# Kernel tuning notes

Measured on AMD Instinct MI355X. Metric: run time of the kernel, lower is better.

The kernel has to match this reference:

```python
import jax, jax.numpy as jnp
import numpy as np

IN_DIM = 1024
OUT_DIM = 1024
QK_DIM = OUT_DIM // 4  # 256


def setup_inputs() -> dict:
    key = jax.random.key(0)
    kx, ky, kq, kk, kv = jax.random.split(key, 5)
    B, Sq, Sk = 16, 2048, 2048
    x = jax.random.normal(kx, (B, Sq, IN_DIM), dtype=jnp.float32)
    y = jax.random.normal(ky, (B, Sk, IN_DIM), dtype=jnp.float32)
    s = 1.0 / np.sqrt(IN_DIM)
    Wq = jax.random.normal(kq, (IN_DIM, QK_DIM), dtype=jnp.float32) * s
    Wk = jax.random.normal(kk, (IN_DIM, QK_DIM), dtype=jnp.float32) * s
    Wv = jax.random.normal(kv, (IN_DIM, OUT_DIM), dtype=jnp.float32) * s
    return {"x": x, "y": y, "Wq": Wq, "Wk": Wk, "Wv": Wv}


def reference(x, y, Wq, Wk, Wv):
    # q: [B,Sq,dk], k: [B,Sk,dk]
    q = jnp.einsum("bsd,dk->bsk", x, Wq)
    k = jnp.einsum("btd,dk->btk", y, Wk)
    # NOTE: original scales by out_dim**0.5, not qk dim
    scores = jnp.einsum("bsk,btk->bst", q, k) / jnp.sqrt(jnp.float32(OUT_DIM))
    attn = jax.nn.softmax(scores, axis=-1)
    v = jnp.einsum("btd,de->bte", y, Wv)
    out = jnp.einsum("bst,bte->bse", attn, v)
    return out + x
```

## Files before the change

### kernel.cpp

```cpp
#include <hip/hip_runtime.h>

typedef __attribute__((ext_vector_type(8))) short bf16x8;
typedef __attribute__((ext_vector_type(4))) short s16x4;
typedef __attribute__((ext_vector_type(4))) float f32x4;

#define MFMA16(a,b,c) __builtin_amdgcn_mfma_f32_16x16x32_bf16((a),(b),(c),0,0,0)

__device__ __forceinline__ unsigned short f2bf(float f) {
  unsigned int u = __float_as_uint(f);
  return (unsigned short)((u + 0x7fffu + ((u >> 16) & 1u)) >> 16);
}
__device__ __forceinline__ float bf2f(unsigned short u) {
  return __uint_as_float(((unsigned int)u) << 16);
}

__device__ __forceinline__ void gload16(const void* g, void* l) {
  __builtin_amdgcn_global_load_lds((const __attribute__((address_space(1))) void*)g,
                                   (__attribute__((address_space(3))) void*)l, 16, 0, 0);
}

__global__ __launch_bounds__(256) void cvt_bf16(const float* __restrict__ in,
                                                unsigned short* __restrict__ out, int n8) {
  for (int i = blockIdx.x * 256 + threadIdx.x; i < n8; i += gridDim.x * 256) {
    float4 a = ((const float4*)in)[2 * i];
    float4 b = ((const float4*)in)[2 * i + 1];
    s16x4 p0, p1;
    p0[0] = f2bf(a.x); p0[1] = f2bf(a.y); p0[2] = f2bf(a.z); p0[3] = f2bf(a.w);
    p1[0] = f2bf(b.x); p1[1] = f2bf(b.y); p1[2] = f2bf(b.z); p1[3] = f2bf(b.w);
    ((s16x4*)out)[2 * i] = p0;
    ((s16x4*)out)[2 * i + 1] = p1;
  }
}

__global__ __launch_bounds__(256) void tcvt(const float* __restrict__ W,
                                            unsigned short* __restrict__ Wt, int K, int N) {
  __shared__ float t[32][33];
  const int n0 = blockIdx.x * 32, k0 = blockIdx.y * 32;
  const int c = threadIdx.x & 31, r8 = threadIdx.x >> 5;
#pragma unroll
  for (int p = 0; p < 4; ++p) {
    int r = r8 + p * 8;
    t[r][c] = W[(size_t)(k0 + r) * N + n0 + c];
  }
  __syncthreads();
#pragma unroll
  for (int p = 0; p < 4; ++p) {
    int r = r8 + p * 8;
    Wt[(size_t)(n0 + r) * K + k0 + c] = f2bf(t[c][r]);
  }
}

__global__ __launch_bounds__(256) void proj_gemm(
    const unsigned short* __restrict__ A, const unsigned short* __restrict__ Bt,
    void* __restrict__ Cv, int N, int mode, float scale)
{
  __shared__ __align__(16) unsigned short As[2][4096];
  __shared__ __align__(16) unsigned short Bs[2][4096];
  const int tid = threadIdx.x, lane = tid & 63, w = tid >> 6;
  const int wr = w >> 1, wc = w & 1;
  const int lrow = lane & 15, lg = lane >> 4;
  const size_t bm = (size_t)blockIdx.x * 128;
  const size_t bn = (size_t)blockIdx.y * 128;
  const int rl = lane >> 2, cq = lane & 3;

  auto stage = [&](int kt, int buf) {
#pragma unroll
    for (int u = 0; u < 2; ++u) {
      int row = w * 32 + u * 16 + rl;
      gload16(A  + (bm + row) * 1024 + kt * 32 + cq * 8, &As[buf][(w * 32 + u * 16) * 32]);
      gload16(Bt + (bn + row) * 1024 + kt * 32 + cq * 8, &Bs[buf][(w * 32 + u * 16) * 32]);
    }
  };

  f32x4 acc[4][4] = {};
  stage(0, 0);
  __syncthreads();

  for (int kt = 0; kt < 32; ++kt) {
    const int cur = kt & 1;
    if (kt + 1 < 32) stage(kt + 1, cur ^ 1);
    bf16x8 af[4], bfr[4];
#pragma unroll
    for (int i = 0; i < 4; ++i)
      af[i] = *(const bf16x8*)&As[cur][(wr * 64 + i * 16 + lrow) * 32 + lg * 8];
#pragma unroll
    for (int j = 0; j < 4; ++j)
      bfr[j] = *(const bf16x8*)&Bs[cur][(wc * 64 + j * 16 + lrow) * 32 + lg * 8];
    __builtin_amdgcn_s_setprio(1);
#pragma unroll
    for (int i = 0; i < 4; ++i)
#pragma unroll
      for (int j = 0; j < 4; ++j)
        acc[i][j] = MFMA16(af[i], bfr[j], acc[i][j]);
    __builtin_amdgcn_s_setprio(0);
    __syncthreads();
  }

  const int orow0 = blockIdx.x * 128 + wr * 64;
  const int ocol0 = blockIdx.y * 128 + wc * 64;
  if (mode == 0) {
    unsigned short* C = (unsigned short*)Cv;
#pragma unroll
    for (int i = 0; i < 4; ++i)
#pragma unroll
      for (int j = 0; j < 4; ++j) {
        int col = ocol0 + j * 16 + lrow;
#pragma unroll
        for (int r = 0; r < 4; ++r) {
          int row = orow0 + i * 16 + lg * 4 + r;
          C[(size_t)row * N + col] = f2bf(acc[i][j][r] * scale);
        }
      }
  } else {
    unsigned char* C8 = (unsigned char*)Cv;
#pragma unroll
    for (int i = 0; i < 4; ++i) {
      int m0 = orow0 + i * 16 + lg * 4;
      int bb = m0 >> 11, t = m0 & 2047;
      int tw = t >> 6, t64 = t & 63;
#pragma unroll
      for (int j = 0; j < 4; ++j) {
        int e = ocol0 + j * 16 + lrow;
        int eg = e >> 4;
        int pk = 0;
        pk = __builtin_amdgcn_cvt_pk_fp8_f32(acc[i][j][0], acc[i][j][1], pk, false);
        pk = __builtin_amdgcn_cvt_pk_fp8_f32(acc[i][j][2], acc[i][j][3], pk, true);
        *(unsigned int*)(C8 + (size_t)bb * 2097152
                            + ((size_t)(eg * 32 + tw)) * 1024 + lrow * 64 + t64)
            = (unsigned int)pk;
      }
    }
  }
}

#define SBAR  do { __builtin_amdgcn_s_barrier(); __builtin_amdgcn_sched_barrier(0); } while (0)

template<int NT, int NTIL, int MODE>
__global__ __launch_bounds__(512) void gemm4p(
    const unsigned short* __restrict__ Aall, const unsigned short* __restrict__ Ball,
    size_t abatch, size_t bbatch, int lda, int ldb,
    unsigned short* __restrict__ Cb, const float* __restrict__ X,
    float* __restrict__ Out, int b0, int nb)
{
  __shared__ __align__(16) unsigned short lds[65536];
  const int bid = blockIdx.x;
  const int bloc = bid % nb, tl = bid / nb;
  const int mtile = tl / NTIL, ntile = tl % NTIL;
  const int gb = b0 + bloc;
  const unsigned short* Ag = Aall + (MODE == 0 ? (size_t)gb : (size_t)bloc) * abatch
                                  + (size_t)mtile * 256 * lda;
  const unsigned short* Bg = Ball + (size_t)gb * bbatch + (size_t)ntile * 256 * ldb;

  const int tid = threadIdx.x, lane = tid & 63, w = tid >> 6;
  const int wm = w >> 2, wn = w & 3;
  const int lrow = lane & 15, lg = lane >> 4;
  char* lb = (char*)lds;

  auto stageU = [&](const unsigned short* G, int ld, int kofs, int ubyte) {
#pragma unroll
    for (int i = 0; i < 2; ++i) {
      int c = tid + 512 * i;
      int row = c >> 2, q = c & 3;
      int qs = q ^ ((row >> 1) & 3);
      gload16(G + (size_t)row * ld + kofs + qs * 8, lb + ubyte + c * 16);
    }
  };
  auto rdfrag = [&](int ubyte, int row) -> bf16x8 {
    return *(const bf16x8*)(lb + ubyte + row * 64 + ((lg ^ ((row >> 1) & 3)) << 4));
  };

  f32x4 acc[8][4] = {};
  bf16x8 afA[4], afB[4], bfrA[4], bfrB[4];

  stageU(Ag, lda, 0,  (0 * 2 + 0) * 16384);
  stageU(Bg, ldb, 0,  (1 * 2 + 0) * 16384);
  stageU(Ag, lda, 32, (2 * 2 + 0) * 16384);
  stageU(Bg, ldb, 32, (3 * 2 + 0) * 16384);
  stageU(Ag, lda, 64, (0 * 2 + 1) * 16384);
  stageU(Bg, ldb, 64, (1 * 2 + 1) * 16384);
  asm volatile("s_waitcnt vmcnt(8)" ::: "memory");
  SBAR;
#pragma unroll
  for (int i = 0; i < 4; ++i) afA[i] = rdfrag(0, wm * 128 + i * 16 + lrow);
#pragma unroll
  for (int nf = 0; nf < 4; ++nf) bfrA[nf] = rdfrag(2 * 16384, wn * 64 + nf * 16 + lrow);

  for (int T = 0; T < NT; ++T) {
    const int pc = T & 1, pn = (T + 1) & 1;
    const int a1b = (2 * 2 + pc) * 16384, b1b = (3 * 2 + pc) * 16384;
    const int a0b = (0 * 2 + pc) * 16384;
    const int t1 = (T + 1 < NT) ? T + 1 : 0;
    const int t2 = (T + 2 < NT) ? T + 2 : 0;

#pragma unroll
    for (int i = 0; i < 4; ++i) afB[i] = rdfrag(a0b, wm * 128 + (i + 4) * 16 + lrow);
    stageU(Ag, lda, t1 * 64 + 32, (2 * 2 + pn) * 16384);
    asm volatile("s_waitcnt lgkmcnt(4)" ::: "memory");
    __builtin_amdgcn_sched_barrier(0);
    __builtin_amdgcn_s_setprio(1);
#pragma unroll
    for (int mf = 0; mf < 4; ++mf)
#pragma unroll
      for (int nf = 0; nf < 4; ++nf)
        acc[mf][nf] = MFMA16(afA[mf], bfrA[nf], acc[mf][nf]);
    __builtin_amdgcn_s_setprio(0);
    asm volatile("s_waitcnt vmcnt(6)" ::: "memory");
    SBAR;

#pragma unroll
    for (int i = 0; i < 4; ++i) afA[i] = rdfrag(a1b, wm * 128 + i * 16 + lrow);
#pragma unroll
    for (int nf = 0; nf < 4; ++nf) bfrB[nf] = rdfrag(b1b, wn * 64 + nf * 16 + lrow);
    stageU(Bg, ldb, t1 * 64 + 32, (3 * 2 + pn) * 16384);
    asm volatile("s_waitcnt lgkmcnt(8)" ::: "memory");
    __builtin_amdgcn_sched_barrier(0);
    __builtin_amdgcn_s_setprio(1);
#pragma unroll
    for (int mf = 0; mf < 4; ++mf)
#pragma unroll
      for (int nf = 0; nf < 4; ++nf)
        acc[mf + 4][nf] = MFMA16(afB[mf], bfrA[nf], acc[mf + 4][nf]);
    __builtin_amdgcn_s_setprio(0);
    SBAR;

#pragma unroll
    for (int i = 0; i < 4; ++i) afB[i] = rdfrag(a1b, wm * 128 + (i + 4) * 16 + lrow);
    stageU(Ag, lda, t2 * 64, (0 * 2 + pc) * 16384);
    asm volatile("s_waitcnt lgkmcnt(4)" ::: "memory");
    __builtin_amdgcn_sched_barrier(0);
    __builtin_amdgcn_s_setprio(1);
#pragma unroll
    for (int mf = 0; mf < 4; ++mf)
#pragma unroll
      for (int nf = 0; nf < 4; ++nf)
        acc[mf][nf] = MFMA16(afA[mf], bfrB[nf], acc[mf][nf]);
    __builtin_amdgcn_s_setprio(0);
    asm volatile("s_waitcnt vmcnt(6)" ::: "memory");
    SBAR;

#pragma unroll
    for (int i = 0; i < 4; ++i) afA[i] = rdfrag((0 * 2 + pn) * 16384, wm * 128 + i * 16 + lrow);
#pragma unroll
    for (int nf = 0; nf < 4; ++nf) bfrA[nf] = rdfrag((1 * 2 + pn) * 16384, wn * 64 + nf * 16 + lrow);
    stageU(Bg, ldb, t2 * 64, (1 * 2 + pc) * 16384);
    asm volatile("s_waitcnt lgkmcnt(8)" ::: "memory");
    __builtin_amdgcn_sched_barrier(0);
    __builtin_amdgcn_s_setprio(1);
#pragma unroll
    for (int mf = 0; mf < 4; ++mf)
#pragma unroll
      for (int nf = 0; nf < 4; ++nf)
        acc[mf + 4][nf] = MFMA16(afB[mf], bfrB[nf], acc[mf + 4][nf]);
    __builtin_amdgcn_s_setprio(0);
    SBAR;
  }

  {
    unsigned short* Cp = Cb + (size_t)bloc * 2048 * 2048;
#pragma unroll
    for (int mf = 0; mf < 8; ++mf)
#pragma unroll
      for (int r = 0; r < 4; ++r) {
        int row = mtile * 256 + wm * 128 + mf * 16 + lg * 4 + r;
#pragma unroll
        for (int nf = 0; nf < 4; ++nf) {
          int col = ntile * 256 + wn * 64 + nf * 16 + lrow;
          Cp[(size_t)row * 2048 + col] = f2bf(acc[mf][nf][r]);
        }
      }
  }
  (void)X; (void)Out;
}

__global__ __launch_bounds__(256) void softmax_kernel(
    const unsigned short* __restrict__ Sp, unsigned char* __restrict__ Pp) {
  const int row = blockIdx.x * 4 + (threadIdx.x >> 6);
  const int lane = threadIdx.x & 63;
  const unsigned short* rp = Sp + (size_t)row * 2048;
  bf16x8 raw[4];
#pragma unroll
  for (int c = 0; c < 4; ++c) raw[c] = *(const bf16x8*)(rp + c * 512 + lane * 8);
  float v[32];
#pragma unroll
  for (int c = 0; c < 4; ++c)
#pragma unroll
    for (int j = 0; j < 8; ++j) v[c * 8 + j] = bf2f((unsigned short)raw[c][j]);
  float mx = v[0];
#pragma unroll
  for (int j = 1; j < 32; ++j) mx = fmaxf(mx, v[j]);
  mx = fmaxf(mx, __shfl_xor(mx, 1));
  mx = fmaxf(mx, __shfl_xor(mx, 2));
  mx = fmaxf(mx, __shfl_xor(mx, 4));
  mx = fmaxf(mx, __shfl_xor(mx, 8));
  mx = fmaxf(mx, __shfl_xor(mx, 16));
  mx = fmaxf(mx, __shfl_xor(mx, 32));
  float sum = 0.f;
#pragma unroll
  for (int j = 0; j < 32; ++j) { v[j] = __expf(v[j] - mx); sum += v[j]; }
  sum += __shfl_xor(sum, 1);
  sum += __shfl_xor(sum, 2);
  sum += __shfl_xor(sum, 4);
  sum += __shfl_xor(sum, 8);
  sum += __shfl_xor(sum, 16);
  sum += __shfl_xor(sum, 32);
  const float scale = 64.0f / sum;
  unsigned char* rp8 = Pp + (size_t)row * 2048;
#pragma unroll
  for (int c = 0; c < 4; ++c) {
    int lo = 0, hi = 0;
    lo = __builtin_amdgcn_cvt_pk_fp8_f32(v[c * 8 + 0] * scale, v[c * 8 + 1] * scale, lo, false);
    lo = __builtin_amdgcn_cvt_pk_fp8_f32(v[c * 8 + 2] * scale, v[c * 8 + 3] * scale, lo, true);
    hi = __builtin_amdgcn_cvt_pk_fp8_f32(v[c * 8 + 4] * scale, v[c * 8 + 5] * scale, hi, false);
    hi = __builtin_amdgcn_cvt_pk_fp8_f32(v[c * 8 + 6] * scale, v[c * 8 + 7] * scale, hi, true);
    uint2 o; o.x = (unsigned int)lo; o.y = (unsigned int)hi;
    *(uint2*)(rp8 + c * 512 + lane * 8) = o;
  }
}

__global__ __launch_bounds__(512) void pvf8_kernel(
    const unsigned char* __restrict__ Pp,
    const unsigned char* __restrict__ Vp,
    const float* __restrict__ X, float* __restrict__ Out,
    int b0, int nb)
{
  __shared__ __align__(16) unsigned char lds[4][16384];
  const int bloc = blockIdx.x % nb, tl = blockIdx.x / nb;
  const int mtile = tl >> 3, ntile = tl & 7;
  const int gb = b0 + bloc;
  const unsigned char* Ag = Pp + (size_t)bloc * 4194304 + (size_t)mtile * 256 * 2048;
  const unsigned char* Vb = Vp + (size_t)gb * 2097152;
  const int NT = 32;
  const int tid = threadIdx.x, lane = tid & 63, w = tid >> 6;
  const int wm = w >> 2, wn = w & 3;
  const int lrow = lane & 15, lg = lane >> 4;

  auto stageA = [&](int jt) {
    unsigned char* dst = lds[jt & 3];
#pragma unroll
    for (int i = 0; i < 2; ++i) {
      int c = tid + 512 * i; int row = c >> 2; int q = (c & 3) ^ ((row >> 1) & 3);
      gload16(Ag + (size_t)row * 2048 + jt * 64 + q * 16, dst + c * 16);
    }
  };

  f32x4 acc[8][2] = {};
  stageA(0); stageA(1); stageA(2);
  asm volatile("s_waitcnt vmcnt(4)" ::: "memory");

  for (int jt = 0; jt < NT; ++jt) {
    __builtin_amdgcn_s_barrier();
    long2 bv[2];
#pragma unroll
    for (int nf = 0; nf < 2; ++nf) {
      int eg = ntile * 8 + wn * 2 + nf;
      bv[nf] = *(const long2*)(Vb + ((size_t)(eg * 32 + jt)) * 1024 + lrow * 64 + lg * 16);
    }
    if (jt + 3 < NT) stageA(jt + 3);
    const unsigned char* Ab = lds[jt & 3];
    {
      long2 av[4];
#pragma unroll
      for (int mf = 0; mf < 4; ++mf) {
        int row = wm * 128 + mf * 16 + lrow;
        av[mf] = *(const long2*)(Ab + row * 64 + ((lg ^ ((row >> 1) & 3)) << 4));
      }
      __builtin_amdgcn_s_setprio(1);
#pragma unroll
      for (int mf = 0; mf < 4; ++mf)
#pragma unroll
        for (int nf = 0; nf < 2; ++nf) {
          acc[mf][nf] = __builtin_amdgcn_mfma_f32_16x16x32_fp8_fp8(av[mf].x, bv[nf].x, acc[mf][nf], 0, 0, 0);
          acc[mf][nf] = __builtin_amdgcn_mfma_f32_16x16x32_fp8_fp8(av[mf].y, bv[nf].y, acc[mf][nf], 0, 0, 0);
        }
      __builtin_amdgcn_s_setprio(0);
    }
    {
      long2 av[4];
#pragma unroll
      for (int mf = 0; mf < 4; ++mf) {
        int row = wm * 128 + (mf + 4) * 16 + lrow;
        av[mf] = *(const long2*)(Ab + row * 64 + ((lg ^ ((row >> 1) & 3)) << 4));
      }
      __builtin_amdgcn_s_setprio(1);
#pragma unroll
      for (int mf = 0; mf < 4; ++mf)
#pragma unroll
        for (int nf = 0; nf < 2; ++nf) {
          acc[mf + 4][nf] = __builtin_amdgcn_mfma_f32_16x16x32_fp8_fp8(av[mf].x, bv[nf].x, acc[mf + 4][nf], 0, 0, 0);
          acc[mf + 4][nf] = __builtin_amdgcn_mfma_f32_16x16x32_fp8_fp8(av[mf].y, bv[nf].y, acc[mf + 4][nf], 0, 0, 0);
        }
      __builtin_amdgcn_s_setprio(0);
    }
  }

#pragma unroll
  for (int mf = 0; mf < 8; ++mf)
#pragma unroll
    for (int r = 0; r < 4; ++r) {
      int row = mtile * 256 + wm * 128 + mf * 16 + lg * 4 + r;
      const float* xr = X   + ((size_t)gb * 2048 + row) * 1024;
      float*      orp = Out + ((size_t)gb * 2048 + row) * 1024;
#pragma unroll
      for (int nf = 0; nf < 2; ++nf) {
        int col = ntile * 128 + wn * 32 + nf * 16 + lrow;
        orp[col] = acc[mf][nf][r] * 0.015625f + xr[col];
      }
    }
}

extern "C" void kernel_launch(void* const* d_in, const int* in_sizes, int n_in,
                              void* d_out, int out_size, void* d_ws, size_t ws_size,
                              hipStream_t stream) {
  (void)in_sizes; (void)n_in; (void)out_size;
  const float* x  = (const float*)d_in[0];
  const float* y  = (const float*)d_in[1];
  const float* Wq = (const float*)d_in[2];
  const float* Wk = (const float*)d_in[3];
  const float* Wv = (const float*)d_in[4];
  float* out = (float*)d_out;

  unsigned short* xb = (unsigned short*)d_out;
  unsigned short* yb = xb + (size_t)16 * 2048 * 1024;

  char* p = (char*)d_ws;
  unsigned short* Wqt = (unsigned short*)p;  p += (size_t)256 * 1024 * 2;
  unsigned short* Wkt = (unsigned short*)p;  p += (size_t)256 * 1024 * 2;
  unsigned short* Wvt = (unsigned short*)p;  p += (size_t)1024 * 1024 * 2;
  unsigned short* qws = (unsigned short*)p;  p += (size_t)16 * 2048 * 256 * 2;
  unsigned short* kws = (unsigned short*)p;  p += (size_t)16 * 2048 * 256 * 2;
  unsigned char*  vp8 = (unsigned char*)p;   p += (size_t)16 * 1024 * 2048;
  char* dyn = p;
  const size_t fixed_bytes = (size_t)(dyn - (char*)d_ws);
  const size_t per_batch = (size_t)2048 * 2048 * 2 + (size_t)2048 * 2048;
  int nb = 1;
  if      (ws_size >= fixed_bytes + 16 * per_batch) nb = 16;
  else if (ws_size >= fixed_bytes + 8  * per_batch) nb = 8;
  else if (ws_size >= fixed_bytes + 4  * per_batch) nb = 4;
  else if (ws_size >= fixed_bytes + 2  * per_batch) nb = 2;
  else nb = 1;
  unsigned short* Sp = (unsigned short*)dyn;
  unsigned char*  Pp = (unsigned char*)(dyn + (size_t)nb * 2048 * 2048 * 2);

  const int n8 = (16 * 2048 * 1024) / 8;
  cvt_bf16<<<2048, 256, 0, stream>>>(x, xb, n8);
  cvt_bf16<<<2048, 256, 0, stream>>>(y, yb, n8);
  tcvt<<<dim3(8, 32),  256, 0, stream>>>(Wq, Wqt, 1024, 256);
  tcvt<<<dim3(8, 32),  256, 0, stream>>>(Wk, Wkt, 1024, 256);
  tcvt<<<dim3(32, 32), 256, 0, stream>>>(Wv, Wvt, 1024, 1024);

  proj_gemm<<<dim3(256, 2), 256, 0, stream>>>(xb, Wqt, (void*)qws, 256, 0, 0.03125f);
  proj_gemm<<<dim3(256, 2), 256, 0, stream>>>(yb, Wkt, (void*)kws, 256, 0, 1.0f);
  proj_gemm<<<dim3(256, 8), 256, 0, stream>>>(yb, Wvt, (void*)vp8, 1024, 2, 1.0f);

  for (int b0 = 0; b0 < 16; b0 += nb) {
    gemm4p<4, 8, 0><<<nb * 64, 512, 0, stream>>>(
        qws, kws, (size_t)2048 * 256, (size_t)2048 * 256, 256, 256,
        Sp, nullptr, nullptr, b0, nb);
    softmax_kernel<<<nb * 512, 256, 0, stream>>>(Sp, Pp);
    pvf8_kernel<<<nb * 64, 512, 0, stream>>>(Pp, vp8, x, out, b0, nb);
  }
}
```

Measured before the change: 494.9 us.

## Route V projection through 256x256 gemm4p tile and triple-buffer PV kernel

```diff
diff --git a/kernel.cpp b/kernel.cpp
--- a/kernel.cpp
+++ b/kernel.cpp
@@ -52,7 +52,7 @@
 
 __global__ __launch_bounds__(256) void proj_gemm(
     const unsigned short* __restrict__ A, const unsigned short* __restrict__ Bt,
-    void* __restrict__ Cv, int N, int mode, float scale)
+    unsigned short* __restrict__ C, int N, float scale)
 {
   __shared__ __align__(16) unsigned short As[2][4096];
   __shared__ __align__(16) unsigned short Bs[2][4096];
@@ -98,39 +98,17 @@
 
   const int orow0 = blockIdx.x * 128 + wr * 64;
   const int ocol0 = blockIdx.y * 128 + wc * 64;
-  if (mode == 0) {
-    unsigned short* C = (unsigned short*)Cv;
-#pragma unroll
-    for (int i = 0; i < 4; ++i)
-#pragma unroll
-      for (int j = 0; j < 4; ++j) {
-        int col = ocol0 + j * 16 + lrow;
-#pragma unroll
-        for (int r = 0; r < 4; ++r) {
-          int row = orow0 + i * 16 + lg * 4 + r;
-          C[(size_t)row * N + col] = f2bf(acc[i][j][r] * scale);
-        }
-      }
-  } else {
-    unsigned char* C8 = (unsigned char*)Cv;
-#pragma unroll
-    for (int i = 0; i < 4; ++i) {
-      int m0 = orow0 + i * 16 + lg * 4;
-      int bb = m0 >> 11, t = m0 & 2047;
-      int tw = t >> 6, t64 = t & 63;
-#pragma unroll
-      for (int j = 0; j < 4; ++j) {
-        int e = ocol0 + j * 16 + lrow;
-        int eg = e >> 4;
-        int pk = 0;
-        pk = __builtin_amdgcn_cvt_pk_fp8_f32(acc[i][j][0], acc[i][j][1], pk, false);
-        pk = __builtin_amdgcn_cvt_pk_fp8_f32(acc[i][j][2], acc[i][j][3], pk, true);
-        *(unsigned int*)(C8 + (size_t)bb * 2097152
-                            + ((size_t)(eg * 32 + tw)) * 1024 + lrow * 64 + t64)
-            = (unsigned int)pk;
-      }
-    }
-  }
+#pragma unroll
+  for (int i = 0; i < 4; ++i)
+#pragma unroll
+    for (int j = 0; j < 4; ++j) {
+      int col = ocol0 + j * 16 + lrow;
+#pragma unroll
+      for (int r = 0; r < 4; ++r) {
+        int row = orow0 + i * 16 + lg * 4 + r;
+        C[(size_t)row * N + col] = f2bf(acc[i][j][r] * scale);
+      }
+    }
 }
 
 #define SBAR  do { __builtin_amdgcn_s_barrier(); __builtin_amdgcn_sched_barrier(0); } while (0)
@@ -139,8 +117,7 @@
 __global__ __launch_bounds__(512) void gemm4p(
     const unsigned short* __restrict__ Aall, const unsigned short* __restrict__ Ball,
     size_t abatch, size_t bbatch, int lda, int ldb,
-    unsigned short* __restrict__ Cb, const float* __restrict__ X,
-    float* __restrict__ Out, int b0, int nb)
+    unsigned short* __restrict__ Cb, int b0, int nb)
 {
   __shared__ __align__(16) unsigned short lds[65536];
   const int bid = blockIdx.x;
@@ -255,7 +232,7 @@
     SBAR;
   }
 
-  {
+  if (MODE == 0) {
     unsigned short* Cp = Cb + (size_t)bloc * 2048 * 2048;
 #pragma unroll
     for (int mf = 0; mf < 8; ++mf)
@@ -268,8 +245,26 @@
           Cp[(size_t)row * 2048 + col] = f2bf(acc[mf][nf][r]);
         }
       }
-  }
-  (void)X; (void)Out;
+  } else {
+    unsigned char* C8 = (unsigned char*)Cb;
+#pragma unroll
+    for (int mf = 0; mf < 8; ++mf) {
+      int m0 = mtile * 256 + wm * 128 + mf * 16 + lg * 4;
+      int bb = m0 >> 11, t = m0 & 2047;
+      int tw = t >> 6, t64 = t & 63;
+#pragma unroll
+      for (int nf = 0; nf < 4; ++nf) {
+        int e = ntile * 256 + wn * 64 + nf * 16 + lrow;
+        int eg = e >> 4;
+        int pk = 0;
+        pk = __builtin_amdgcn_cvt_pk_fp8_f32(acc[mf][nf][0], acc[mf][nf][1], pk, false);
+        pk = __builtin_amdgcn_cvt_pk_fp8_f32(acc[mf][nf][2], acc[mf][nf][3], pk, true);
+        *(unsigned int*)(C8 + (size_t)bb * 2097152
+                            + ((size_t)(eg * 32 + tw)) * 1024 + lrow * 64 + t64)
+            = (unsigned int)pk;
+      }
+    }
+  }
 }
 
 __global__ __launch_bounds__(256) void softmax_kernel(
@@ -317,13 +312,13 @@
   }
 }
 
-__global__ __launch_bounds__(512) void pvf8_kernel(
+__global__ __launch_bounds__(512, 6) void pvf8_kernel(
     const unsigned char* __restrict__ Pp,
     const unsigned char* __restrict__ Vp,
     const float* __restrict__ X, float* __restrict__ Out,
     int b0, int nb)
 {
-  __shared__ __align__(16) unsigned char lds[4][16384];
+  __shared__ __align__(16) unsigned char lds[3][16384];
   const int bloc = blockIdx.x % nb, tl = blockIdx.x / nb;
   const int mtile = tl >> 3, ntile = tl & 7;
   const int gb = b0 + bloc;
@@ -335,7 +330,7 @@
   const int lrow = lane & 15, lg = lane >> 4;
 
   auto stageA = [&](int jt) {
-    unsigned char* dst = lds[jt & 3];
+    unsigned char* dst = lds[jt % 3];
 #pragma unroll
     for (int i = 0; i < 2; ++i) {
       int c = tid + 512 * i; int row = c >> 2; int q = (c & 3) ^ ((row >> 1) & 3);
@@ -344,8 +339,8 @@
   };
 
   f32x4 acc[8][2] = {};
-  stageA(0); stageA(1); stageA(2);
-  asm volatile("s_waitcnt vmcnt(4)" ::: "memory");
+  stageA(0); stageA(1);
+  asm volatile("s_waitcnt vmcnt(2)" ::: "memory");
 
   for (int jt = 0; jt < NT; ++jt) {
     __builtin_amdgcn_s_barrier();
@@ -355,8 +350,8 @@
       int eg = ntile * 8 + wn * 2 + nf;
       bv[nf] = *(const long2*)(Vb + ((size_t)(eg * 32 + jt)) * 1024 + lrow * 64 + lg * 16);
     }
-    if (jt + 3 < NT) stageA(jt + 3);
-    const unsigned char* Ab = lds[jt & 3];
+    if (jt + 2 < NT) stageA(jt + 2);
+    const unsigned char* Ab = lds[jt % 3];
     {
       long2 av[4];
 #pragma unroll
@@ -448,14 +443,15 @@
   tcvt<<<dim3(8, 32),  256, 0, stream>>>(Wk, Wkt, 1024, 256);
   tcvt<<<dim3(32, 32), 256, 0, stream>>>(Wv, Wvt, 1024, 1024);
 
-  proj_gemm<<<dim3(256, 2), 256, 0, stream>>>(xb, Wqt, (void*)qws, 256, 0, 0.03125f);
-  proj_gemm<<<dim3(256, 2), 256, 0, stream>>>(yb, Wkt, (void*)kws, 256, 0, 1.0f);
-  proj_gemm<<<dim3(256, 8), 256, 0, stream>>>(yb, Wvt, (void*)vp8, 1024, 2, 1.0f);
+  proj_gemm<<<dim3(256, 2), 256, 0, stream>>>(xb, Wqt, qws, 256, 0.03125f);
+  proj_gemm<<<dim3(256, 2), 256, 0, stream>>>(yb, Wkt, kws, 256, 1.0f);
+  gemm4p<16, 4, 2><<<512, 512, 0, stream>>>(
+      yb, Wvt, 0, 0, 1024, 1024, (unsigned short*)vp8, 0, 1);
 
   for (int b0 = 0; b0 < 16; b0 += nb) {
     gemm4p<4, 8, 0><<<nb * 64, 512, 0, stream>>>(
         qws, kws, (size_t)2048 * 256, (size_t)2048 * 256, 256, 256,
-        Sp, nullptr, nullptr, b0, nb);
+        Sp, b0, nb);
     softmax_kernel<<<nb * 512, 256, 0, stream>>>(Sp, Pp);
     pvf8_kernel<<<nb * 64, 512, 0, stream>>>(Pp, vp8, x, out, b0, nb);
   }
```

Measured after the change: 809.8 us. +63.6%, slower.
